# Performance work log

Hardware: AMD Instinct MI355X
Metric: run time of the kernel (lower is better)

Reference implementation:

```python
import jax, jax.numpy as jnp
import numpy as np

B, L, E = 4, 2048, 1024
H, DH = 16, 64          # num_heads, head_dim; hidden = H*DH = 1024
HID = H * DH
EPS = 1e-5


def setup_inputs() -> dict:
    key = jax.random.key(0)
    ks = jax.random.split(key, 16)
    s = 0.02
    return {
        "emb": jax.random.normal(ks[0], (B, L, E), jnp.float32),
        "Wa": jax.random.normal(ks[1], (H, E, DH), jnp.float32) * s,
        "ba": jax.random.normal(ks[2], (H, DH), jnp.float32) * s,
        "Wb": jax.random.normal(ks[3], (H, E, DH), jnp.float32) * s,
        "bb": jax.random.normal(ks[4], (H, DH), jnp.float32) * s,
        "WD": jax.random.normal(ks[5], (H, E, DH), jnp.float32) * s,
        "bD": jax.random.normal(ks[6], (H, DH), jnp.float32) * s,
        "WC": jax.random.normal(ks[7], (H, DH, DH), jnp.float32) * s,
        "bC": jax.random.normal(ks[8], (H, DH), jnp.float32) * s,
        "ffn1_w": jax.random.normal(ks[9], (HID, 4 * HID), jnp.float32) * s,
        "ffn1_b": jnp.zeros((4 * HID,), jnp.float32),
        "ffn2_w": jax.random.normal(ks[10], (4 * HID, HID), jnp.float32) * s,
        "ffn2_b": jnp.zeros((HID,), jnp.float32),
        "proj_w": jax.random.normal(ks[11], (HID, HID), jnp.float32) * s,
        "proj_b": jnp.zeros((HID,), jnp.float32),
        "ln_g": jnp.ones((HID,), jnp.float32),
        "ln_b": jnp.zeros((HID,), jnp.float32),
    }


def _layernorm(x, g, b):
    mu = jnp.mean(x, -1, keepdims=True)
    var = jnp.mean(jnp.square(x - mu), -1, keepdims=True)
    return (x - mu) * jax.lax.rsqrt(var + EPS) * g + b


def reference(emb, Wa, ba, Wb, bb, WD, bD, WC, bC,
              ffn1_w, ffn1_b, ffn2_w, ffn2_b, proj_w, proj_b, ln_g, ln_b):
    # per-head gates/inputs for all timesteps at once: [B, L, H, DH]
    a = jnp.tanh(jnp.einsum('ble,hed->blhd', emb, Wa) + ba)
    b = jnp.einsum('ble,hed->blhd', emb, Wb) + bb

    # affine recurrence h_t = a_t * h_{t-1} + b_t, h_0 = 0 -> parallel scan over L
    def comb(c1, c2):
        a1, b1 = c1
        a2, b2 = c2
        return a1 * a2, a2 * b1 + b2

    _, h = jax.lax.associative_scan(comb, (a, b), axis=1)  # [B, L, H, DH]

    d = jnp.einsum('ble,hed->blhd', emb, WD) + bD
    head_out = (jnp.einsum('blhd,hdf->blhf', h, WC) + bC) * d  # [B, L, H, DH]
    z = head_out.reshape(B, L, HID)

    u = z + _layernorm(z, ln_g, ln_b)
    ffn = jax.nn.gelu(u @ ffn1_w + ffn1_b, approximate=False) @ ffn2_w + ffn2_b
    return (u + ffn) @ proj_w + proj_b
```

## Files before the change

### kernel.cpp

```cpp
#include <hip/hip_runtime.h>
#include <hip/hip_bf16.h>
#include <math.h>

#define B_   4
#define L_   2048
#define E_   1024
#define H_   16
#define DH_  64
#define HID_ 1024
#define ROWS (B_*L_)
#define NCH  16
#define CLEN (L_/NCH)

typedef __attribute__((ext_vector_type(8))) short short8;
typedef __attribute__((ext_vector_type(4))) float f32x4;

__device__ __forceinline__ unsigned short f2bf(float f) {
  union { float f; unsigned int i; } v; v.f = f;
  unsigned int r = v.i + 0x7fffu + ((v.i >> 16) & 1u);
  return (unsigned short)(r >> 16);
}
__device__ __forceinline__ float bf2f(unsigned int u) {
  union { unsigned int i; float f; } v; v.i = u << 16; return v.f;
}

__device__ __forceinline__ void gload16(const unsigned short* g, unsigned short* l) {
  __builtin_amdgcn_global_load_lds((const __attribute__((address_space(1))) void*)g,
                                   (__attribute__((address_space(3))) void*)l, 16, 0, 0);
}

__global__ void cast_f32_bf16(const float* __restrict__ src, unsigned short* __restrict__ dst, int n) {
  int i = (blockIdx.x * 256 + threadIdx.x) * 4;
  if (i < n) {
    float4 v = *(const float4*)(src + i);
    ushort4 o;
    o.x = f2bf(v.x); o.y = f2bf(v.y); o.z = f2bf(v.z); o.w = f2bf(v.w);
    *(ushort4*)(dst + i) = o;
  }
}

__global__ void transpose_cast(const float* __restrict__ src, unsigned short* __restrict__ dst,
                               int R, int C, int dstBase) {
  __shared__ float tile[32][33];
  src += (size_t)blockIdx.z * R * C;
  int dstRow0 = dstBase + blockIdx.z * C;
  int rb = blockIdx.x * 32, cb = blockIdx.y * 32;
  for (int i = threadIdx.y; i < 32; i += 8)
    tile[i][threadIdx.x] = src[(size_t)(rb + i) * C + cb + threadIdx.x];
  __syncthreads();
  for (int i = threadIdx.y; i < 32; i += 8)
    dst[(size_t)(dstRow0 + cb + i) * R + rb + threadIdx.x] = f2bf(tile[threadIdx.x][i]);
}

__global__ void build_bias(const float* __restrict__ ba, const float* __restrict__ bb,
                           const float* __restrict__ bD, float* __restrict__ bias) {
  int i = blockIdx.x * 256 + threadIdx.x;
  const float* src = (i < 1024) ? ba : ((i < 2048) ? bb : bD);
  bias[i] = src[i & 1023];
}

__global__ void build_wcd(const float* __restrict__ WC, unsigned short* __restrict__ dst) {
  int i = blockIdx.x * 256 + threadIdx.x;
  int c = i >> 7, kl = i & 127;
  float v = ((kl >> 6) == ((c >> 6) & 1)) ? WC[(size_t)(c >> 6) * 4096 + (kl & 63) * 64 + (c & 63)] : 0.f;
  dst[i] = f2bf(v);
}

#define EPI_GATES 0
#define EPI_GELU  1
#define EPI_RES   2
#define EPI_OUT   3
#define EPI_HEAD  4

template<int EPI>
__device__ __forceinline__ void epi_store(float xa, int rr, int cc, int N,
                                          const float* __restrict__ bias,
                                          const void* __restrict__ aux,
                                          void* __restrict__ out, void* __restrict__ out2) {
  float x = xa + bias[cc];
  if (EPI == EPI_GATES) {
    if (cc < HID_) {
      x = tanhf(x);
      ((unsigned short*)out)[(size_t)rr * 2048 + (cc << 1)] = f2bf(x);
    } else if (cc < 2048) {
      ((unsigned short*)out)[(size_t)rr * 2048 + ((cc - 1024) << 1) + 1] = f2bf(x);
    } else {
      ((unsigned short*)out2)[(size_t)rr * 1024 + (cc - 2048)] = f2bf(x);
    }
  } else if (EPI == EPI_GELU) {
    x = 0.5f * x * (1.f + erff(x * 0.70710678118654752f));
    ((unsigned short*)out)[(size_t)rr * N + cc] = f2bf(x);
  } else if (EPI == EPI_RES) {
    x += ((const float*)aux)[(size_t)rr * N + cc];
    ((unsigned short*)out)[(size_t)rr * N + cc] = f2bf(x);
  } else if (EPI == EPI_HEAD) {
    x *= bf2f(((const unsigned short*)aux)[(size_t)rr * 1024 + cc]);
    ((float*)out)[(size_t)rr * N + cc] = x;
  } else {
    ((float*)out)[(size_t)rr * N + cc] = x;
  }
}

template<int EPI, int DIAG>
__global__ __launch_bounds__(256)
void gemm_bt(const unsigned short* __restrict__ A, int lda,
             const unsigned short* __restrict__ Bt, int ldb,
             const float* __restrict__ bias, const void* __restrict__ aux,
             void* __restrict__ out, void* __restrict__ out2, int M, int N, int K) {
  __shared__ unsigned short lA[128 * 32];
  __shared__ unsigned short lB[128 * 32];
  const int tid = threadIdx.x;
  const int w = tid >> 6, l = tid & 63;
  const int gx = gridDim.x, nwg = gx * gridDim.y;
  const int o = blockIdx.y * gx + blockIdx.x;
  const int lin = (o & 7) * (nwg >> 3) + (o >> 3);
  const int row0 = (lin / gx) * 128, col0 = (lin % gx) * 128;
  const int kOff = DIAG ? col0 : 0;

  const int rA0 = w * 16 + (l >> 2);
  const int rA1 = (4 + w) * 16 + (l >> 2);
  const int koff = (l & 3) * 8;
  const unsigned short* gA0 = A + (size_t)(row0 + rA0) * lda + kOff + koff;
  const unsigned short* gA1 = A + (size_t)(row0 + rA1) * lda + kOff + koff;
  const unsigned short* gB0 = Bt + (size_t)(col0 + rA0) * ldb + koff;
  const unsigned short* gB1 = Bt + (size_t)(col0 + rA1) * ldb + koff;
  unsigned short* lA0 = lA + w * 512;
  unsigned short* lA1 = lA + (4 + w) * 512;
  unsigned short* lB0 = lB + w * 512;
  unsigned short* lB1 = lB + (4 + w) * 512;

  const int wr = (w >> 1) * 64, wc = (w & 1) * 64;
  f32x4 acc[4][4];
  #pragma unroll
  for (int m = 0; m < 4; m++)
    #pragma unroll
    for (int n = 0; n < 4; n++) acc[m][n] = (f32x4){0.f, 0.f, 0.f, 0.f};

  const int arow = wr + (l & 15);
  const int brow = wc + (l & 15);
  const int kg = (l >> 4) * 8;

  for (int kt = 0; kt < K; kt += 32) {
    __syncthreads();
    gload16(gA0 + kt, lA0);
    gload16(gA1 + kt, lA1);
    gload16(gB0 + kt, lB0);
    gload16(gB1 + kt, lB1);
    __syncthreads();
    short8 af[4], bfr[4];
    #pragma unroll
    for (int m = 0; m < 4; m++) af[m]  = *(const short8*)(lA + (arow + m * 16) * 32 + kg);
    #pragma unroll
    for (int n = 0; n < 4; n++) bfr[n] = *(const short8*)(lB + (brow + n * 16) * 32 + kg);
    #pragma unroll
    for (int m = 0; m < 4; m++)
      #pragma unroll
      for (int n = 0; n < 4; n++)
        acc[m][n] = __builtin_amdgcn_mfma_f32_16x16x32_bf16(af[m], bfr[n], acc[m][n], 0, 0, 0);
  }

  const int er = row0 + wr + ((l >> 4) << 2);
  const int ec = col0 + wc + (l & 15);
  #pragma unroll
  for (int m = 0; m < 4; m++)
    #pragma unroll
    for (int n = 0; n < 4; n++)
      #pragma unroll
      for (int j = 0; j < 4; j++)
        epi_store<EPI>(acc[m][n][j], er + m * 16 + j, ec + n * 16, N, bias, aux, out, out2);
}

template<int EPI>
__global__ __launch_bounds__(512, 2)
void gemm256(const unsigned short* __restrict__ A, const unsigned short* __restrict__ Bt,
             const float* __restrict__ bias, const void* __restrict__ aux,
             void* __restrict__ out, void* __restrict__ out2, int M, int N, int K) {
  __shared__ unsigned short lds[2][2][256 * 64];
  const int tid = threadIdx.x;
  const int w = tid >> 6, l = tid & 63;
  const int wm = w >> 2, wn = w & 3;
  const int gx = gridDim.x, nwg = gx * gridDim.y;
  const int o = blockIdx.y * gx + blockIdx.x;
  const int lin = (o & 7) * (nwg >> 3) + (o >> 3);
  const int row0 = (lin / gx) * 256, col0 = (lin % gx) * 256;
  const int lr = l & 15, kg = (l >> 4) << 3;
  const int wmb = wm * 128, wnb = wn * 64;
  const int nIter = K >> 7;

  const int srow = w * 8 + (l >> 3);
  const int kswz = (((l & 7) ^ (l >> 3)) << 3);

  f32x4 acc[8][4];
  #pragma unroll
  for (int m = 0; m < 8; m++)
    #pragma unroll
    for (int n = 0; n < 4; n++) acc[m][n] = (f32x4){0.f, 0.f, 0.f, 0.f};

  short8 a[4][2], b0[2][2], b1[2][2];

  auto stA = [&](int buf, int hh, int kt) {
    const unsigned short* g = A + (size_t)(row0 + hh * 128 + srow) * K + kt * 64 + kswz;
    unsigned short* d = &lds[buf][0][hh * 8192 + w * 512];
    gload16(g, d);
    gload16(g + (size_t)64 * K, d + 4096);
  };
  auto stB = [&](int buf, int hh, int kt) {
    const unsigned short* g = Bt + (size_t)(col0 + hh * 128 + srow) * K + kt * 64 + kswz;
    unsigned short* d = &lds[buf][1][hh * 8192 + w * 512];
    gload16(g, d);
    gload16(g + (size_t)64 * K, d + 4096);
  };

#define RD_A(LP, mh) { _Pragma("unroll") for (int mf = 0; mf < 4; ++mf) { _Pragma("unroll") for (int ks = 0; ks < 2; ++ks) { \
      int r = wmb + (mh) * 64 + mf * 16 + lr; int k = ks * 32 + kg; \
      a[mf][ks] = *(const short8*)((LP) + r * 64 + (k ^ ((r & 7) << 3))); } } }
#define RD_B(dst, LP, nh) { _Pragma("unroll") for (int nf = 0; nf < 2; ++nf) { _Pragma("unroll") for (int ks = 0; ks < 2; ++ks) { \
      int r = wnb + (nh) * 32 + nf * 16 + lr; int k = ks * 32 + kg; \
      dst[nf][ks] = *(const short8*)((LP) + r * 64 + (k ^ ((r & 7) << 3))); } } }
#define MMA(bb, MB, NB) \
    __builtin_amdgcn_s_setprio(1); \
    _Pragma("unroll") for (int mf = 0; mf < 4; ++mf) { _Pragma("unroll") for (int nf = 0; nf < 2; ++nf) { _Pragma("unroll") for (int ks = 0; ks < 2; ++ks) { \
      acc[(MB) + mf][(NB) + nf] = __builtin_amdgcn_mfma_f32_16x16x32_bf16(a[mf][ks], bb[nf][ks], acc[(MB) + mf][(NB) + nf], 0, 0, 0); } } } \
    __builtin_amdgcn_s_setprio(0);

  stA(0, 0, 0); stA(0, 1, 0); stB(0, 0, 0); stB(0, 1, 0);
  stB(1, 0, 1); stA(1, 0, 1);
  asm volatile("s_waitcnt vmcnt(4)" ::: "memory");
  __builtin_amdgcn_s_barrier();

  for (int i = 0; i < nIter; ++i) {
    const int t0 = 2 * i, t1 = t0 + 1;
    const bool pf = (i + 1 < nIter);
    const unsigned short* LA0 = lds[0][0];
    const unsigned short* LB0 = lds[0][1];
    const unsigned short* LA1 = lds[1][0];
    const unsigned short* LB1 = lds[1][1];

    RD_A(LA0, 0); RD_B(b0, LB0, 0);
    stA(1, 1, t1); stB(1, 1, t1);
    __builtin_amdgcn_s_barrier();
    MMA(b0, 0, 0);
    __builtin_amdgcn_s_barrier();
    RD_B(b1, LB0, 1);
    __builtin_amdgcn_s_barrier();
    MMA(b1, 0, 2);
    __builtin_amdgcn_s_barrier();
    RD_A(LA0, 1);
    if (pf) stB(0, 0, t0 + 2);
    __builtin_amdgcn_s_barrier();
    MMA(b0, 4, 0);
    __builtin_amdgcn_s_barrier();
    if (pf) stA(0, 0, t0 + 2);
    if (pf) asm volatile("s_waitcnt vmcnt(4)" ::: "memory");
    else    asm volatile("s_waitcnt vmcnt(0)" ::: "memory");
    __builtin_amdgcn_s_barrier();
    MMA(b1, 4, 2);
    __builtin_amdgcn_s_barrier();

    RD_A(LA1, 0); RD_B(b0, LB1, 0);
    if (pf) { stA(0, 1, t0 + 2); stB(0, 1, t0 + 2); }
    __builtin_amdgcn_s_barrier();
    MMA(b0, 0, 0);
    __builtin_amdgcn_s_barrier();
    RD_B(b1, LB1, 1);
    __builtin_amdgcn_s_barrier();
    MMA(b1, 0, 2);
    __builtin_amdgcn_s_barrier();
    RD_A(LA1, 1);
    if (pf) stB(1, 0, t1 + 2);
    __builtin_amdgcn_s_barrier();
    MMA(b0, 4, 0);
    __builtin_amdgcn_s_barrier();
    if (pf) stA(1, 0, t1 + 2);
    if (pf) asm volatile("s_waitcnt vmcnt(4)" ::: "memory");
    else    asm volatile("s_waitcnt vmcnt(0)" ::: "memory");
    __builtin_amdgcn_s_barrier();
    MMA(b1, 4, 2);
    __builtin_amdgcn_s_barrier();
  }
#undef RD_A
#undef RD_B
#undef MMA

  const int er = row0 + wmb + ((l >> 4) << 2);
  const int ec = col0 + wnb + lr;
  #pragma unroll
  for (int mi = 0; mi < 8; ++mi)
    #pragma unroll
    for (int ni = 0; ni < 4; ++ni)
      #pragma unroll
      for (int j = 0; j < 4; ++j)
        epi_store<EPI>(acc[mi][ni][j], er + mi * 16 + j, ec + ni * 16, N, bias, aux, out, out2);
}

template<int EPI>
__global__ __launch_bounds__(512, 2)
void gemm256x128(const unsigned short* __restrict__ A, const unsigned short* __restrict__ Bt,
                 const float* __restrict__ bias, const void* __restrict__ aux,
                 void* __restrict__ out, void* __restrict__ out2, int M, int N, int K) {
  __shared__ unsigned short lA2[2][256 * 64];
  __shared__ unsigned short lB2[2][128 * 64];
  const int tid = threadIdx.x;
  const int w = tid >> 6, l = tid & 63;
  const int wm = w >> 1, wn = w & 1;
  const int gx = gridDim.x, nwg = gx * gridDim.y;
  const int o = blockIdx.y * gx + blockIdx.x;
  const int lin = (o & 7) * (nwg >> 3) + (o >> 3);
  const int row0 = (lin / gx) * 256, col0 = (lin % gx) * 128;
  const int lr = l & 15, kg = (l >> 4) << 3;
  const int nIter = K >> 7;

  const int srow = w * 8 + (l >> 3);
  const int kswz = (((l & 7) ^ (l >> 3)) << 3);

  f32x4 acc[4][4];
  #pragma unroll
  for (int m = 0; m < 4; m++)
    #pragma unroll
    for (int n = 0; n < 4; n++) acc[m][n] = (f32x4){0.f, 0.f, 0.f, 0.f};

  short8 a[2][2], b0[2][2], b1[2][2];

  auto stA = [&](int buf, int hh, int kt) {
    const unsigned short* g = A + (size_t)(row0 + hh * 128 + srow) * K + kt * 64 + kswz;
    unsigned short* d = &lA2[buf][hh * 8192 + w * 512];
    gload16(g, d);
    gload16(g + (size_t)64 * K, d + 4096);
  };
  auto stB = [&](int buf, int hh, int kt) {
    const unsigned short* g = Bt + (size_t)(col0 + hh * 64 + srow) * K + kt * 64 + kswz;
    gload16(g, &lB2[buf][hh * 4096 + w * 512]);
  };

#define RDA2(buf, mh) { _Pragma("unroll") for (int mf = 0; mf < 2; ++mf) { _Pragma("unroll") for (int ks = 0; ks < 2; ++ks) { \
      int r = wm * 64 + (mh) * 32 + mf * 16 + lr; int k = ks * 32 + kg; \
      a[mf][ks] = *(const short8*)(&lA2[buf][r * 64 + (k ^ ((r & 7) << 3))]); } } }
#define RDB2(dst, buf, nh) { _Pragma("unroll") for (int nf = 0; nf < 2; ++nf) { _Pragma("unroll") for (int ks = 0; ks < 2; ++ks) { \
      int r = wn * 64 + (nh) * 32 + nf * 16 + lr; int k = ks * 32 + kg; \
      dst[nf][ks] = *(const short8*)(&lB2[buf][r * 64 + (k ^ ((r & 7) << 3))]); } } }
#define MMA2(bb, MB, NB) \
    __builtin_amdgcn_s_setprio(1); \
    _Pragma("unroll") for (int mf = 0; mf < 2; ++mf) { _Pragma("unroll") for (int nf = 0; nf < 2; ++nf) { _Pragma("unroll") for (int ks = 0; ks < 2; ++ks) { \
      acc[(MB) + mf][(NB) + nf] = __builtin_amdgcn_mfma_f32_16x16x32_bf16(a[mf][ks], bb[nf][ks], acc[(MB) + mf][(NB) + nf], 0, 0, 0); } } } \
    __builtin_amdgcn_s_setprio(0);

  stA(0, 0, 0); stA(0, 1, 0); stB(0, 0, 0); stB(0, 1, 0);
  stB(1, 0, 1); stA(1, 0, 1);
  asm volatile("s_waitcnt vmcnt(3)" ::: "memory");
  __builtin_amdgcn_s_barrier();

  for (int i = 0; i < nIter; ++i) {
    const int t0 = 2 * i, t1 = t0 + 1;
    const bool pf = (i + 1 < nIter);

    RDA2(0, 0); RDB2(b0, 0, 0);
    stA(1, 1, t1); stB(1, 1, t1);
    __builtin_amdgcn_s_barrier();
    MMA2(b0, 0, 0);
    __builtin_amdgcn_s_barrier();
    RDB2(b1, 0, 1);
    __builtin_amdgcn_s_barrier();
    MMA2(b1, 0, 2);
    __builtin_amdgcn_s_barrier();
    RDA2(0, 1);
    if (pf) stB(0, 0, t0 + 2);
    __builtin_amdgcn_s_barrier();
    MMA2(b0, 2, 0);
    __builtin_amdgcn_s_barrier();
    if (pf) stA(0, 0, t0 + 2);
    if (pf) asm volatile("s_waitcnt vmcnt(3)" ::: "memory");
    else    asm volatile("s_waitcnt vmcnt(0)" ::: "memory");
    __builtin_amdgcn_s_barrier();
    MMA2(b1, 2, 2);
    __builtin_amdgcn_s_barrier();

    RDA2(1, 0); RDB2(b0, 1, 0);
    if (pf) { stA(0, 1, t0 + 2); stB(0, 1, t0 + 2); }
    __builtin_amdgcn_s_barrier();
    MMA2(b0, 0, 0);
    __builtin_amdgcn_s_barrier();
    RDB2(b1, 1, 1);
    __builtin_amdgcn_s_barrier();
    MMA2(b1, 0, 2);
    __builtin_amdgcn_s_barrier();
    RDA2(1, 1);
    if (pf) stB(1, 0, t1 + 2);
    __builtin_amdgcn_s_barrier();
    MMA2(b0, 2, 0);
    __builtin_amdgcn_s_barrier();
    if (pf) stA(1, 0, t1 + 2);
    if (pf) asm volatile("s_waitcnt vmcnt(3)" ::: "memory");
    else    asm volatile("s_waitcnt vmcnt(0)" ::: "memory");
    __builtin_amdgcn_s_barrier();
    MMA2(b1, 2, 2);
    __builtin_amdgcn_s_barrier();
  }
#undef RDA2
#undef RDB2
#undef MMA2

  const int er = row0 + wm * 64 + ((l >> 4) << 2);
  const int ec = col0 + wn * 64 + lr;
  #pragma unroll
  for (int mi = 0; mi < 4; ++mi)
    #pragma unroll
    for (int ni = 0; ni < 4; ++ni)
      #pragma unroll
      for (int j = 0; j < 4; ++j)
        epi_store<EPI>(acc[mi][ni][j], er + mi * 16 + j, ec + ni * 16, N, bias, aux, out, out2);
}

__global__ void scan_p1(const unsigned short* __restrict__ ab16, float* __restrict__ aggA, float* __restrict__ aggB) {
  int id = blockIdx.x * 256 + threadIdx.x;
  int c = id & 1023;
  int chunk = (id >> 10) & (NCH - 1);
  int bb = id >> 14;
  const unsigned short* base = ab16 + (size_t)(bb * L_ + chunk * CLEN) * 2048 + 2 * c;
  float Aa = 1.f, Bv = 0.f;
  #pragma unroll 4
  for (int t = 0; t < CLEN; ++t) {
    unsigned int v = *(const unsigned int*)(base + (size_t)t * 2048);
    float a = bf2f(v & 0xffffu);
    float b = bf2f(v >> 16);
    Aa *= a;
    Bv = a * Bv + b;
  }
  int o = (chunk * B_ + bb) * 1024 + c;
  aggA[o] = Aa; aggB[o] = Bv;
}

__global__ void scan_p2(const float* __restrict__ aggA, const float* __restrict__ aggB,
                        float* __restrict__ hinit) {
  int id = blockIdx.x * 256 + threadIdx.x;
  float hc = 0.f;
  for (int ch = 0; ch < NCH; ++ch) {
    int o = ch * 4096 + id;
    hinit[o] = hc;
    hc = aggA[o] * hc + aggB[o];
  }
}

__global__ void scan_p3(const unsigned short* __restrict__ ab16, const float* __restrict__ hinit,
                        unsigned short* __restrict__ hb16) {
  int id = blockIdx.x * 256 + threadIdx.x;
  int c = id & 1023;
  int chunk = (id >> 10) & (NCH - 1);
  int bb = id >> 14;
  const unsigned short* base = ab16 + (size_t)(bb * L_ + chunk * CLEN) * 2048 + 2 * c;
  unsigned short* hb = hb16 + (size_t)(bb * L_ + chunk * CLEN) * 1024;
  float h = hinit[chunk * 4096 + bb * 1024 + c];
  #pragma unroll 4
  for (int t = 0; t < CLEN; ++t) {
    unsigned int v = *(const unsigned int*)(base + (size_t)t * 2048);
    float a = bf2f(v & 0xffffu);
    float b = bf2f(v >> 16);
    h = a * h + b;
    hb[(size_t)t * 1024 + c] = f2bf(h);
  }
}

__global__ __launch_bounds__(256)
void ln_res(const float* __restrict__ z, const float* __restrict__ lg, const float* __restrict__ lb,
            float* __restrict__ u32, unsigned short* __restrict__ u16) {
  int row = blockIdx.x;
  int t = threadIdx.x;
  const float4 zv = *(const float4*)(z + (size_t)row * 1024 + t * 4);
  float s = zv.x + zv.y + zv.z + zv.w;
  float sq = zv.x * zv.x + zv.y * zv.y + zv.z * zv.z + zv.w * zv.w;
  #pragma unroll
  for (int o = 32; o > 0; o >>= 1) { s += __shfl_down(s, o); sq += __shfl_down(sq, o); }
  __shared__ float ps[4], pq[4];
  if ((t & 63) == 0) { ps[t >> 6] = s; pq[t >> 6] = sq; }
  __syncthreads();
  s = ps[0] + ps[1] + ps[2] + ps[3];
  sq = pq[0] + pq[1] + pq[2] + pq[3];
  float mu = s * (1.f / 1024.f);
  float var = sq * (1.f / 1024.f) - mu * mu;
  float rs = rsqrtf(var + 1e-5f);
  const float4 gv = *(const float4*)(lg + t * 4);
  const float4 bv = *(const float4*)(lb + t * 4);
  float4 o;
  o.x = zv.x + (zv.x - mu) * rs * gv.x + bv.x;
  o.y = zv.y + (zv.y - mu) * rs * gv.y + bv.y;
  o.z = zv.z + (zv.z - mu) * rs * gv.z + bv.z;
  o.w = zv.w + (zv.w - mu) * rs * gv.w + bv.w;
  *(float4*)(u32 + (size_t)row * 1024 + t * 4) = o;
  ushort4 ob; ob.x = f2bf(o.x); ob.y = f2bf(o.y); ob.z = f2bf(o.z); ob.w = f2bf(o.w);
  *(ushort4*)(u16 + (size_t)row * 1024 + t * 4) = ob;
}

extern "C" void kernel_launch(void* const* d_in, const int* in_sizes, int n_in,
                              void* d_out, int out_size, void* d_ws, size_t ws_size,
                              hipStream_t stream) {
  const float* emb    = (const float*)d_in[0];
  const float* Wa     = (const float*)d_in[1];
  const float* ba     = (const float*)d_in[2];
  const float* Wb     = (const float*)d_in[3];
  const float* bb     = (const float*)d_in[4];
  const float* WD     = (const float*)d_in[5];
  const float* bD     = (const float*)d_in[6];
  const float* WC     = (const float*)d_in[7];
  const float* bC     = (const float*)d_in[8];
  const float* ffn1_w = (const float*)d_in[9];
  const float* ffn1_b = (const float*)d_in[10];
  const float* ffn2_w = (const float*)d_in[11];
  const float* ffn2_b = (const float*)d_in[12];
  const float* proj_w = (const float*)d_in[13];
  const float* proj_b = (const float*)d_in[14];
  const float* ln_g   = (const float*)d_in[15];
  const float* ln_b   = (const float*)d_in[16];

  char* p = (char*)d_ws;
  auto alloc = [&](size_t bytes) { char* r = p; p += (bytes + 255) & ~(size_t)255; return (void*)r; };

  unsigned short* ab16 = (unsigned short*)alloc((size_t)ROWS * 2048 * 2);
  unsigned short* d16  = (unsigned short*)alloc((size_t)ROWS * 1024 * 2);
  unsigned short* hb16 = (unsigned short*)alloc((size_t)ROWS * 1024 * 2);
  float* zbuf  = (float*)alloc((size_t)ROWS * 1024 * 4);
  float* u32   = (float*)alloc((size_t)ROWS * 1024 * 4);
  unsigned short* u16  = (unsigned short*)alloc((size_t)ROWS * 1024 * 2);
  unsigned short* embb = (unsigned short*)alloc((size_t)ROWS * 1024 * 2);
  unsigned short* wcat = (unsigned short*)alloc((size_t)3072 * 1024 * 2);
  unsigned short* f1t  = (unsigned short*)alloc((size_t)4096 * 1024 * 2);
  unsigned short* f2t  = (unsigned short*)alloc((size_t)4096 * 1024 * 2);
  unsigned short* pjt  = (unsigned short*)alloc((size_t)1024 * 1024 * 2);
  unsigned short* wcd  = (unsigned short*)alloc((size_t)1024 * 128 * 2);
  float* biascat = (float*)alloc(3072 * 4);
  float* aggA  = (float*)alloc(65536 * 4);
  float* aggB  = (float*)alloc(65536 * 4);
  float* hinit = (float*)alloc(65536 * 4);
  unsigned short* gbuf = ab16;
  unsigned short* vbuf = (unsigned short*)zbuf;

  dim3 tb(32, 8);
  cast_f32_bf16<<<ROWS * 1024 / 1024, 256, 0, stream>>>(emb, embb, ROWS * 1024);
  build_bias<<<12, 256, 0, stream>>>(ba, bb, bD, biascat);
  build_wcd<<<1024 * 128 / 256, 256, 0, stream>>>(WC, wcd);
  transpose_cast<<<dim3(E_ / 32, DH_ / 32, H_), tb, 0, stream>>>(Wa, wcat, E_, DH_, 0);
  transpose_cast<<<dim3(E_ / 32, DH_ / 32, H_), tb, 0, stream>>>(Wb, wcat, E_, DH_, 1024);
  transpose_cast<<<dim3(E_ / 32, DH_ / 32, H_), tb, 0, stream>>>(WD, wcat, E_, DH_, 2048);
  transpose_cast<<<dim3(1024 / 32, 4096 / 32, 1), tb, 0, stream>>>(ffn1_w, f1t, 1024, 4096, 0);
  transpose_cast<<<dim3(4096 / 32, 1024 / 32, 1), tb, 0, stream>>>(ffn2_w, f2t, 4096, 1024, 0);
  transpose_cast<<<dim3(1024 / 32, 1024 / 32, 1), tb, 0, stream>>>(proj_w, pjt, 1024, 1024, 0);

  gemm256<EPI_GATES><<<dim3(3072 / 256, ROWS / 256), 512, 0, stream>>>(
      embb, wcat, biascat, nullptr, ab16, d16, ROWS, 3072, 1024);

  scan_p1<<<65536 / 256, 256, 0, stream>>>(ab16, aggA, aggB);
  scan_p2<<<4096 / 256, 256, 0, stream>>>(aggA, aggB, hinit);
  scan_p3<<<65536 / 256, 256, 0, stream>>>(ab16, hinit, hb16);

  gemm_bt<EPI_HEAD, 1><<<dim3(1024 / 128, ROWS / 128), 256, 0, stream>>>(
      hb16, 1024, wcd, 128, bC, d16, zbuf, nullptr, ROWS, 1024, 128);

  ln_res<<<ROWS, 256, 0, stream>>>(zbuf, ln_g, ln_b, u32, u16);

  gemm256<EPI_GELU><<<dim3(4096 / 256, ROWS / 256), 512, 0, stream>>>(
      u16, f1t, ffn1_b, nullptr, gbuf, nullptr, ROWS, 4096, 1024);
  gemm256x128<EPI_RES><<<dim3(1024 / 128, ROWS / 256), 512, 0, stream>>>(
      gbuf, f2t, ffn2_b, u32, vbuf, nullptr, ROWS, 1024, 4096);
  gemm256x128<EPI_OUT><<<dim3(1024 / 128, ROWS / 256), 512, 0, stream>>>(
      vbuf, pjt, proj_b, nullptr, (float*)d_out, nullptr, ROWS, 1024, 1024);
}
```

Baseline: 553.9 us.

## Restructure GEMM prefetch to load whole k-tiles per buffer; use 256x128 for gates

Changes the double-buffered pipeline in both GEMM kernels. Each buffer now receives a full k-tile (both halves of A and B) at points where that buffer has already been consumed, replacing the staggered half-tile loads, and the vmcnt waits are adjusted to match. The gate-projection GEMM also switches from the 256x256 tile kernel to the 256x128 kernel, which doubles its grid size. The aim is fewer stalls and better occupancy or wave count, at the cost of a shorter prefetch distance per buffer and more A re-reads. The second-half wait in the loop no longer has a vmcnt(0) fallback on the final iteration, so that path relies on the first-half wait having drained outstanding loads.

```diff
diff --git a/kernel.cpp b/kernel.cpp
--- a/kernel.cpp
+++ b/kernel.cpp
@@ -222,14 +222,15 @@
     _Pragma("unroll") for (int mf = 0; mf < 4; ++mf) { _Pragma("unroll") for (int nf = 0; nf < 2; ++nf) { _Pragma("unroll") for (int ks = 0; ks < 2; ++ks) { \
       acc[(MB) + mf][(NB) + nf] = __builtin_amdgcn_mfma_f32_16x16x32_bf16(a[mf][ks], bb[nf][ks], acc[(MB) + mf][(NB) + nf], 0, 0, 0); } } } \
     __builtin_amdgcn_s_setprio(0);
+#define BAR __builtin_amdgcn_s_barrier()
 
   stA(0, 0, 0); stA(0, 1, 0); stB(0, 0, 0); stB(0, 1, 0);
-  stB(1, 0, 1); stA(1, 0, 1);
-  asm volatile("s_waitcnt vmcnt(4)" ::: "memory");
-  __builtin_amdgcn_s_barrier();
+  stA(1, 0, 1); stA(1, 1, 1); stB(1, 0, 1); stB(1, 1, 1);
+  asm volatile("s_waitcnt vmcnt(8)" ::: "memory");
+  BAR;
 
   for (int i = 0; i < nIter; ++i) {
-    const int t0 = 2 * i, t1 = t0 + 1;
+    const int t2 = 2 * i + 2, t3 = 2 * i + 3;
     const bool pf = (i + 1 < nIter);
     const unsigned short* LA0 = lds[0][0];
     const unsigned short* LB0 = lds[0][1];
@@ -237,46 +238,27 @@
     const unsigned short* LB1 = lds[1][1];
 
     RD_A(LA0, 0); RD_B(b0, LB0, 0);
-    stA(1, 1, t1); stB(1, 1, t1);
-    __builtin_amdgcn_s_barrier();
-    MMA(b0, 0, 0);
-    __builtin_amdgcn_s_barrier();
+    BAR; MMA(b0, 0, 0); BAR;
     RD_B(b1, LB0, 1);
-    __builtin_amdgcn_s_barrier();
-    MMA(b1, 0, 2);
-    __builtin_amdgcn_s_barrier();
+    BAR; MMA(b1, 0, 2); BAR;
     RD_A(LA0, 1);
-    if (pf) stB(0, 0, t0 + 2);
-    __builtin_amdgcn_s_barrier();
-    MMA(b0, 4, 0);
-    __builtin_amdgcn_s_barrier();
-    if (pf) stA(0, 0, t0 + 2);
-    if (pf) asm volatile("s_waitcnt vmcnt(4)" ::: "memory");
-    else    asm volatile("s_waitcnt vmcnt(0)" ::: "memory");
-    __builtin_amdgcn_s_barrier();
-    MMA(b1, 4, 2);
-    __builtin_amdgcn_s_barrier();
+    if (pf) { stB(0, 0, t2); stB(0, 1, t2); }
+    BAR; MMA(b0, 4, 0); BAR;
+    if (pf) { stA(0, 0, t2); stA(0, 1, t2);
+              asm volatile("s_waitcnt vmcnt(8)" ::: "memory"); }
+    else    { asm volatile("s_waitcnt vmcnt(0)" ::: "memory"); }
+    BAR; MMA(b1, 4, 2); BAR;
 
     RD_A(LA1, 0); RD_B(b0, LB1, 0);
-    if (pf) { stA(0, 1, t0 + 2); stB(0, 1, t0 + 2); }
-    __builtin_amdgcn_s_barrier();
-    MMA(b0, 0, 0);
-    __builtin_amdgcn_s_barrier();
+    BAR; MMA(b0, 0, 0); BAR;
     RD_B(b1, LB1, 1);
-    __builtin_amdgcn_s_barrier();
-    MMA(b1, 0, 2);
-    __builtin_amdgcn_s_barrier();
+    BAR; MMA(b1, 0, 2); BAR;
     RD_A(LA1, 1);
-    if (pf) stB(1, 0, t1 + 2);
-    __builtin_amdgcn_s_barrier();
-    MMA(b0, 4, 0);
-    __builtin_amdgcn_s_barrier();
-    if (pf) stA(1, 0, t1 + 2);
-    if (pf) asm volatile("s_waitcnt vmcnt(4)" ::: "memory");
-    else    asm volatile("s_waitcnt vmcnt(0)" ::: "memory");
-    __builtin_amdgcn_s_barrier();
-    MMA(b1, 4, 2);
-    __builtin_amdgcn_s_barrier();
+    if (pf) { stB(1, 0, t3); stB(1, 1, t3); }
+    BAR; MMA(b0, 4, 0); BAR;
+    if (pf) { stA(1, 0, t3); stA(1, 1, t3);
+              asm volatile("s_waitcnt vmcnt(8)" ::: "memory"); }
+    BAR; MMA(b1, 4, 2); BAR;
   }
 #undef RD_A
 #undef RD_B
@@ -343,57 +325,39 @@
     _Pragma("unroll") for (int mf = 0; mf < 2; ++mf) { _Pragma("unroll") for (int nf = 0; nf < 2; ++nf) { _Pragma("unroll") for (int ks = 0; ks < 2; ++ks) { \
       acc[(MB) + mf][(NB) + nf] = __builtin_amdgcn_mfma_f32_16x16x32_bf16(a[mf][ks], bb[nf][ks], acc[(MB) + mf][(NB) + nf], 0, 0, 0); } } } \
     __builtin_amdgcn_s_setprio(0);
+#define BAR2 __builtin_amdgcn_s_barrier()
 
   stA(0, 0, 0); stA(0, 1, 0); stB(0, 0, 0); stB(0, 1, 0);
-  stB(1, 0, 1); stA(1, 0, 1);
-  asm volatile("s_waitcnt vmcnt(3)" ::: "memory");
-  __builtin_amdgcn_s_barrier();
+  stA(1, 0, 1); stA(1, 1, 1); stB(1, 0, 1); stB(1, 1, 1);
+  asm volatile("s_waitcnt vmcnt(6)" ::: "memory");
+  BAR2;
 
   for (int i = 0; i < nIter; ++i) {
-    const int t0 = 2 * i, t1 = t0 + 1;
+    const int t2 = 2 * i + 2, t3 = 2 * i + 3;
     const bool pf = (i + 1 < nIter);
 
     RDA2(0, 0); RDB2(b0, 0, 0);
-    stA(1, 1, t1); stB(1, 1, t1);
-    __builtin_amdgcn_s_barrier();
-    MMA2(b0, 0, 0);
-    __builtin_amdgcn_s_barrier();
+    BAR2; MMA2(b0, 0, 0); BAR2;
     RDB2(b1, 0, 1);
-    __builtin_amdgcn_s_barrier();
-    MMA2(b1, 0, 2);
-    __builtin_amdgcn_s_barrier();
+    BAR2; MMA2(b1, 0, 2); BAR2;
     RDA2(0, 1);
-    if (pf) stB(0, 0, t0 + 2);
-    __builtin_amdgcn_s_barrier();
-    MMA2(b0, 2, 0);
-    __builtin_amdgcn_s_barrier();
-    if (pf) stA(0, 0, t0 + 2);
-    if (pf) asm volatile("s_waitcnt vmcnt(3)" ::: "memory");
-    else    asm volatile("s_waitcnt vmcnt(0)" ::: "memory");
-    __builtin_amdgcn_s_barrier();
-    MMA2(b1, 2, 2);
-    __builtin_amdgcn_s_barrier();
+    if (pf) { stB(0, 0, t2); stB(0, 1, t2); }
+    BAR2; MMA2(b0, 2, 0); BAR2;
+    if (pf) { stA(0, 0, t2); stA(0, 1, t2);
+              asm volatile("s_waitcnt vmcnt(6)" ::: "memory"); }
+    else    { asm volatile("s_waitcnt vmcnt(0)" ::: "memory"); }
+    BAR2; MMA2(b1, 2, 2); BAR2;
 
     RDA2(1, 0); RDB2(b0, 1, 0);
-    if (pf) { stA(0, 1, t0 + 2); stB(0, 1, t0 + 2); }
-    __builtin_amdgcn_s_barrier();
-    MMA2(b0, 0, 0);
-    __builtin_amdgcn_s_barrier();
+    BAR2; MMA2(b0, 0, 0); BAR2;
     RDB2(b1, 1, 1);
-    __builtin_amdgcn_s_barrier();
-    MMA2(b1, 0, 2);
-    __builtin_amdgcn_s_barrier();
+    BAR2; MMA2(b1, 0, 2); BAR2;
     RDA2(1, 1);
-    if (pf) stB(1, 0, t1 + 2);
-    __builtin_amdgcn_s_barrier();
-    MMA2(b0, 2, 0);
-    __builtin_amdgcn_s_barrier();
-    if (pf) stA(1, 0, t1 + 2);
-    if (pf) asm volatile("s_waitcnt vmcnt(3)" ::: "memory");
-    else    asm volatile("s_waitcnt vmcnt(0)" ::: "memory");
-    __builtin_amdgcn_s_barrier();
-    MMA2(b1, 2, 2);
-    __builtin_amdgcn_s_barrier();
+    if (pf) { stB(1, 0, t3); stB(1, 1, t3); }
+    BAR2; MMA2(b0, 2, 0); BAR2;
+    if (pf) { stA(1, 0, t3); stA(1, 1, t3);
+              asm volatile("s_waitcnt vmcnt(6)" ::: "memory"); }
+    BAR2; MMA2(b1, 2, 2); BAR2;
   }
 #undef RDA2
 #undef RDB2
@@ -543,7 +507,7 @@
   transpose_cast<<<dim3(4096 / 32, 1024 / 32, 1), tb, 0, stream>>>(ffn2_w, f2t, 4096, 1024, 0);
   transpose_cast<<<dim3(1024 / 32, 1024 / 32, 1), tb, 0, stream>>>(proj_w, pjt, 1024, 1024, 0);
 
-  gemm256<EPI_GATES><<<dim3(3072 / 256, ROWS / 256), 512, 0, stream>>>(
+  gemm256x128<EPI_GATES><<<dim3(3072 / 128, ROWS / 256), 512, 0, stream>>>(
       embb, wcat, biascat, nullptr, ab16, d16, ROWS, 3072, 1024);
 
   scan_p1<<<65536 / 256, 256, 0, stream>>>(ab16, aggA, aggB);
```

New measurement: 525.7 us. 5.1% less time.
